# Optimization experiments

Measured on AMD Instinct MI355X. Metric: run time of the kernel, lower is better.

The kernel has to match this reference:

```python
import jax, jax.numpy as jnp
import numpy as np

N = 50000      # nodes
E = 800000     # edges (avg degree 16)
DIN = 128
DH = 128
DOUT = 8


def setup_inputs() -> dict:
    key = jax.random.key(0)
    ks = jax.random.split(key, 9)
    def lin(k, o, i):
        return (jax.random.normal(k, (o, i), jnp.float32) / np.sqrt(i)).astype(jnp.float32)
    return {
        "x": jax.random.normal(ks[0], (N, DIN), jnp.float32),
        "edge_index": jax.random.randint(ks[1], (2, E), 0, N),
        "edge_attr": jax.random.normal(ks[2], (E, 1), jnp.float32),
        # SAGEConv params: lin_l (applied to mean-aggregated neighbors, with bias)
        # and lin_r (applied to root node, no bias), per PyG defaults.
        "W1l": lin(ks[3], DH, DIN), "b1l": jnp.zeros((DH,), jnp.float32), "W1r": lin(ks[4], DH, DIN),
        "Whl": lin(ks[5], DH, DH),  "bhl": jnp.zeros((DH,), jnp.float32), "Whr": lin(ks[6], DH, DH),
        "W2l": lin(ks[7], DOUT, DH), "b2l": jnp.zeros((DOUT,), jnp.float32), "W2r": lin(ks[8], DOUT, DH),
    }


def _sage_conv(x, src, dst, Wl, bl, Wr, n):
    # mean aggregation of source features onto destination nodes
    s = jax.ops.segment_sum(x[src], dst, num_segments=n)              # [N, d]
    c = jax.ops.segment_sum(jnp.ones((src.shape[0],), x.dtype), dst, num_segments=n)
    agg = s / jnp.maximum(c, 1.0)[:, None]
    return agg @ Wl.T + bl + x @ Wr.T


def reference(x, edge_index, edge_attr, W1l, b1l, W1r, Whl, bhl, Whr, W2l, b2l, W2r):
    # edge_attr is accepted but unused, matching the original forward.
    src, dst = edge_index[0], edge_index[1]
    n = x.shape[0]
    h = jax.nn.relu(_sage_conv(x, src, dst, W1l, b1l, W1r, n))
    # dropout p=0.5 is identity at inference (training=False)
    h = jax.nn.elu(_sage_conv(h, src, dst, Whl, bhl, Whr, n))
    h = _sage_conv(h, src, dst, W2l, b2l, W2r, n)
    return jax.nn.log_softmax(h, axis=1)
```

## Files before the change

### kernel.cpp

```cpp
#include <hip/hip_runtime.h>

typedef unsigned int u32;
typedef unsigned short u16;
typedef short bf16x8 __attribute__((ext_vector_type(8)));
typedef float f32x4 __attribute__((ext_vector_type(4)));

#define NCB 256

__device__ __forceinline__ float bf2f(u16 h) { return __uint_as_float(((u32)h) << 16); }
__device__ __forceinline__ u16 f2bf(float f) {
    u32 u = __float_as_uint(f);
    return (u16)((u + 0x7fffu + ((u >> 16) & 1u)) >> 16);
}

__global__ __launch_bounds__(256) void k_sentinel(u16* out, int n) {
    int i = blockIdx.x * 256 + threadIdx.x;
    if (i < n) out[i] = f2bf(-7.0f);
}

__global__ void k_detect(const u32* x, int* flag) {
    int lane = threadIdx.x;
    int c = 0;
    for (int j = 0; j < 4; ++j) {
        u32 u = x[lane * 4 + j];
        u32 e = (u >> 7) & 0xffu;
        if ((e >= 0x30u && e <= 0x47u) || ((u & 0x7fffu) == 0u)) ++c;
    }
    for (int d = 32; d; d >>= 1) c += __shfl_down(c, d, 64);
    if (lane == 0) *flag = (c < 128) ? 1 : 0;
}

__global__ __launch_bounds__(256) void k_front(
    const void* x, const int* dstv, const int* flag, int bucketed,
    uint4* X, int* C, int E, int N, int chunk, int cvtB,
    const void* s1l, const void* s1r, const void* shl, const void* shr,
    const void* s2l, const void* s2r, const void* sb1, const void* sbh,
    const void* sb2,
    u32* w1l, u32* w1r, u32* whl, u32* whr, u32* w2l, u32* w2r,
    float* bf1, float* bfh, float* bf2) {
    __shared__ int hist[256];
    int b = blockIdx.x, t = threadIdx.x;
    if (b < cvtB) {
        int i = b * 256 + t;
        if (i >= N * 16) return;
        if (*flag) {
            const float4* s = (const float4*)x;
            float4 a = s[2 * i], c4 = s[2 * i + 1];
            uint4 o;
            o.x = (u32)f2bf(a.x) | ((u32)f2bf(a.y) << 16);
            o.y = (u32)f2bf(a.z) | ((u32)f2bf(a.w) << 16);
            o.z = (u32)f2bf(c4.x) | ((u32)f2bf(c4.y) << 16);
            o.w = (u32)f2bf(c4.z) | ((u32)f2bf(c4.w) << 16);
            X[i] = o;
        } else {
            X[i] = ((const uint4*)x)[i];
        }
    } else if (b < cvtB + 134) {
        int bb = b - cvtB;
        int fl = *flag;
        auto cv = [&](const void* src, u32* dst, int base) {
            int i = base + t;
            if (fl) {
                const float* s = (const float*)src;
                dst[i] = (u32)f2bf(s[2 * i]) | ((u32)f2bf(s[2 * i + 1]) << 16);
            } else {
                dst[i] = ((const u32*)src)[i];
            }
        };
        auto cb = [&](const void* src, float* dst, int i) {
            dst[i] = fl ? ((const float*)src)[i] : bf2f(((const u16*)src)[i]);
        };
        if      (bb <  32) cv(s1l, w1l, bb * 256);
        else if (bb <  64) cv(s1r, w1r, (bb - 32) * 256);
        else if (bb <  96) cv(shl, whl, (bb - 64) * 256);
        else if (bb < 128) cv(shr, whr, (bb - 96) * 256);
        else if (bb < 130) cv(s2l, w2l, (bb - 128) * 256);
        else if (bb < 132) cv(s2r, w2r, (bb - 130) * 256);
        else if (bb == 132) {
            if (t < 128) cb(sb1, bf1, t);
            else         cb(sbh, bfh, t - 128);
        } else {
            if (t < 8) cb(sb2, bf2, t);
        }
    } else if (bucketed) {
        int cb2 = b - cvtB - 134;
        hist[t] = 0;
        __syncthreads();
        int e0 = cb2 * chunk;
        int e1 = min(e0 + chunk, E);
        for (int e = e0 + t; e < e1; e += 256) {
            int d = min(max(dstv[e], 0), N - 1);
            atomicAdd(&hist[d >> 8], 1);
        }
        __syncthreads();
        C[cb2 * 256 + t] = hist[t];
    }
}

__global__ __launch_bounds__(256) void k_scanT(int* C, int* T) {
    __shared__ int sm[256];
    int bu = blockIdx.x, t = threadIdx.x;
    int v = C[t * 256 + bu];
    sm[t] = v;
    __syncthreads();
    for (int off = 1; off < 256; off <<= 1) {
        int u = (t >= off) ? sm[t - off] : 0;
        __syncthreads();
        sm[t] += u;
        __syncthreads();
    }
    C[t * 256 + bu] = sm[t] - v;
    if (t == 255) T[bu] = sm[255];
}

__global__ __launch_bounds__(256) void k_scanB(const int* T, int* B, int nbuk) {
    __shared__ int sm[256];
    int t = threadIdx.x;
    int v = (t < nbuk) ? T[t] : 0;
    sm[t] = v;
    __syncthreads();
    for (int off = 1; off < 256; off <<= 1) {
        int u = (t >= off) ? sm[t - off] : 0;
        __syncthreads();
        sm[t] += u;
        __syncthreads();
    }
    B[t] = sm[t] - v;
}

__global__ __launch_bounds__(256) void k_place(const int* srcv, const int* dstv,
                                               const int* C, const int* Bb,
                                               u32* pairs, int E, int N, int chunk) {
    __shared__ int base[256], cnt[256];
    int t = threadIdx.x;
    base[t] = Bb[t] + C[blockIdx.x * 256 + t];
    cnt[t] = 0;
    __syncthreads();
    int e0 = blockIdx.x * chunk;
    int e1 = min(e0 + chunk, E);
    for (int e = e0 + t; e < e1; e += 256) {
        int d = min(max(dstv[e], 0), N - 1);
        int s = min(max(srcv[e], 0), N - 1);
        int b = d >> 8;
        int pos = base[b] + atomicAdd(&cnt[b], 1);
        pos = min(max(pos, 0), E - 1);
        pairs[pos] = ((u32)s << 8) | (u32)(d & 255);
    }
}

__global__ __launch_bounds__(256) void k_fillb2(const u32* pairs, const int* Bb,
                                                const int* T, int* rowptr,
                                                int* adj, int E, int N, int nbuk) {
    int bu = blockIdx.x;
    int n0 = bu << 8;
    int nn = min(N - n0, 256);
    __shared__ int dcnt[256], sm[256], cur[256];
    int t = threadIdx.x;
    dcnt[t] = 0;
    __syncthreads();
    int s0 = min(max(Bb[bu], 0), E);
    int s1 = min(s0 + max(T[bu], 0), E);
    for (int e = s0 + t; e < s1; e += 256) {
        int ld = (int)(pairs[e] & 255u);
        atomicAdd(&dcnt[min(ld, nn - 1)], 1);
    }
    __syncthreads();
    int v = dcnt[t];
    sm[t] = v;
    __syncthreads();
    for (int off = 1; off < 256; off <<= 1) {
        int u = (t >= off) ? sm[t - off] : 0;
        __syncthreads();
        sm[t] += u;
        __syncthreads();
    }
    int excl = sm[t] - v;
    cur[t] = excl;
    if (t < nn) rowptr[n0 + t] = s0 + excl;
    if (bu == nbuk - 1 && t == 0) rowptr[N] = E;
    __syncthreads();
    for (int e = s0 + t; e < s1; e += 256) {
        u32 pc = pairs[e];
        int ld = min((int)(pc & 255u), nn - 1);
        int src = (int)(pc >> 8);
        int slot = atomicAdd(&cur[ld], 1);
        int idx = min(max(s0 + slot, 0), E - 1);
        adj[idx] = src;
    }
}

__global__ __launch_bounds__(256) void k_zero(int* deg, int N) {
    int i = blockIdx.x * 256 + threadIdx.x;
    if (i < N) deg[i] = 0;
}
__global__ __launch_bounds__(256) void k_deg(const int* dstv, int* deg, int E, int N) {
    int e = blockIdx.x * 256 + threadIdx.x;
    if (e >= E) return;
    int d = dstv[e]; d = min(max(d, 0), N - 1);
    atomicAdd(&deg[d], 1);
}
__global__ __launch_bounds__(512) void k_scan1(const int* deg, int* r0,
                                               int* bsums, int N) {
    __shared__ int sm[512];
    int i = blockIdx.x * 512 + threadIdx.x;
    int v = (i < N) ? deg[i] : 0;
    sm[threadIdx.x] = v;
    __syncthreads();
    for (int off = 1; off < 512; off <<= 1) {
        int t = (threadIdx.x >= off) ? sm[threadIdx.x - off] : 0;
        __syncthreads();
        sm[threadIdx.x] += t;
        __syncthreads();
    }
    if (i < N) r0[i] = sm[threadIdx.x] - v;
    if (threadIdx.x == 511) bsums[blockIdx.x] = sm[511];
}
__global__ __launch_bounds__(128) void k_scan2f(int* bsums, int nb) {
    __shared__ int sm[128];
    int v = (threadIdx.x < nb) ? bsums[threadIdx.x] : 0;
    sm[threadIdx.x] = v;
    __syncthreads();
    for (int off = 1; off < 128; off <<= 1) {
        int t = (threadIdx.x >= off) ? sm[threadIdx.x - off] : 0;
        __syncthreads();
        sm[threadIdx.x] += t;
        __syncthreads();
    }
    if (threadIdx.x < nb) bsums[threadIdx.x] = sm[threadIdx.x] - v;
}
__global__ __launch_bounds__(512) void k_scan3f(const int* r0, const int* bsums,
                                                int* rowptr, int N, int E) {
    int i = blockIdx.x * 512 + threadIdx.x;
    if (i < N) rowptr[i] = r0[i] + bsums[blockIdx.x];
    if (i == 0) rowptr[N] = E;
}
__global__ __launch_bounds__(256) void k_fill(const int* srcv, const int* dstv,
                                              const int* rowptr, int* deg,
                                              int* adj, int E, int N) {
    int e = blockIdx.x * 256 + threadIdx.x;
    if (e >= E) return;
    int d = dstv[e]; d = min(max(d, 0), N - 1);
    int slot = atomicSub(&deg[d], 1) - 1;
    int idx = rowptr[d] + slot;
    idx = min(max(idx, 0), E - 1);
    adj[idx] = srcv[e];
}

__device__ __forceinline__ void acc8m(uint4 u, float m, float* s) {
    const u32* pu = (const u32*)&u;
#pragma unroll
    for (int t = 0; t < 4; ++t) {
        s[2 * t]     = fmaf(__uint_as_float(pu[t] << 16), m, s[2 * t]);
        s[2 * t + 1] = fmaf(__uint_as_float(pu[t] & 0xffff0000u), m, s[2 * t + 1]);
    }
}

__global__ __launch_bounds__(256) void k_aggregate(const uint4* F, const int* rowptr,
                                                   const int* adj, uint4* A,
                                                   int N, int E) {
    int wid = (int)((blockIdx.x * 256u + threadIdx.x) >> 6);
    int lane = threadIdx.x & 63;
    if (wid >= N) return;
    int beg = rowptr[wid], end = rowptr[wid + 1];
    beg = min(max(beg, 0), E);
    end = min(max(end, beg), E);
    int g = lane >> 4, l = lane & 15;
    float s[8] = {0.f, 0.f, 0.f, 0.f, 0.f, 0.f, 0.f, 0.f};
    for (int j = beg + g; j < end; j += 16) {
        int i1 = j + 4, i2 = j + 8, i3 = j + 12;
        float m1 = (i1 < end) ? 1.f : 0.f;
        float m2 = (i2 < end) ? 1.f : 0.f;
        float m3 = (i3 < end) ? 1.f : 0.f;
        int a0 = min(max(adj[j], 0), N - 1);
        int a1 = min(max(adj[min(i1, end - 1)], 0), N - 1);
        int a2 = min(max(adj[min(i2, end - 1)], 0), N - 1);
        int a3 = min(max(adj[min(i3, end - 1)], 0), N - 1);
        uint4 u0 = F[(size_t)a0 * 16 + l];
        uint4 u1 = F[(size_t)a1 * 16 + l];
        uint4 u2 = F[(size_t)a2 * 16 + l];
        uint4 u3 = F[(size_t)a3 * 16 + l];
        acc8m(u0, 1.f, s);
        acc8m(u1, m1, s);
        acc8m(u2, m2, s);
        acc8m(u3, m3, s);
    }
#pragma unroll
    for (int k = 0; k < 8; ++k) {
        s[k] += __shfl_xor(s[k], 16, 64);
        s[k] += __shfl_xor(s[k], 32, 64);
    }
    if (g == 0) {
        float inv = 1.f / fmaxf((float)(end - beg), 1.f);
        uint4 r; u32* pr = (u32*)&r;
#pragma unroll
        for (int t = 0; t < 4; ++t)
            pr[t] = (u32)f2bf(s[2 * t] * inv) | ((u32)f2bf(s[2 * t + 1] * inv) << 16);
        A[(size_t)wid * 16 + l] = r;
    }
}

__global__ __launch_bounds__(256) void k_gemm128(const u16* Agg, const u16* Xin,
                                                 const u32* Wl, const u32* Wr,
                                                 const float* bias, u16* Out, int N) {
    __shared__ __align__(16) u16 Wsh[32768];
    int t = threadIdx.x;
#pragma unroll
    for (int i = 0; i < 16; ++i) {
        int f = i * 256 + t;
        int c = f >> 9, s = (f >> 6) & 7, q = (f >> 4) & 3, n = f & 15;
        int o = c * 16 + n;
        int k = s * 32 + q * 8;
        uint4 v;
        if (k < 128) v = *(const uint4*)(Wl + (size_t)o * 64 + (k >> 1));
        else         v = *(const uint4*)(Wr + (size_t)o * 64 + ((k - 128) >> 1));
        *(uint4*)(Wsh + f * 8) = v;
    }
    __syncthreads();

    int tile = blockIdx.x * 4 + (t >> 6);
    int lane = t & 63;
    int m0 = tile * 16;
    if (m0 >= N) return;
    int mrow = min(m0 + (lane & 15), N - 1);
    int kq = (lane >> 4) * 8;

    bf16x8 afrag[8];
#pragma unroll
    for (int s = 0; s < 8; ++s) {
        int k = s * 32 + kq;
        const u16* p = (k < 128) ? (Agg + (size_t)mrow * 128 + k)
                                 : (Xin + (size_t)mrow * 128 + (k - 128));
        afrag[s] = *(const bf16x8*)p;
    }

    f32x4 acc[8];
#pragma unroll
    for (int c = 0; c < 8; ++c) acc[c] = (f32x4){0.f, 0.f, 0.f, 0.f};

    const u16* lbase = Wsh + (lane >> 4) * 128 + (lane & 15) * 8;
#pragma unroll
    for (int c = 0; c < 8; ++c) {
#pragma unroll
        for (int s = 0; s < 8; ++s) {
            bf16x8 b = *(const bf16x8*)(lbase + (c * 8 + s) * 512);
            acc[c] = __builtin_amdgcn_mfma_f32_16x16x32_bf16(afrag[s], b, acc[c], 0, 0, 0);
        }
    }

#pragma unroll
    for (int c = 0; c < 8; ++c) {
        int o = c * 16 + (lane & 15);
        float bv = bias[o];
#pragma unroll
        for (int r = 0; r < 4; ++r) {
            int m = m0 + (lane >> 4) * 4 + r;
            float v = acc[c][r] + bv;
            v = fmaxf(v, 0.f);
            if (m < N) Out[(size_t)m * 128 + o] = f2bf(v);
        }
    }
}

__global__ __launch_bounds__(256) void k_gemm2(const u16* Agg, const u16* Xin,
                                               const u32* Wl, const u32* Wr,
                                               const float* bias,
                                               const u32* W2l, const u32* W2r,
                                               const float* b2,
                                               float* Y, float* R, int N) {
    __shared__ __align__(16) u16 Wsh[32768];
    __shared__ float W2sh[2048];
    int t = threadIdx.x;
#pragma unroll
    for (int i = 0; i < 16; ++i) {
        int f = i * 256 + t;
        int c = f >> 9, s = (f >> 6) & 7, q = (f >> 4) & 3, n = f & 15;
        int o = c * 16 + n;
        int k = s * 32 + q * 8;
        uint4 v;
        if (k < 128) v = *(const uint4*)(Wl + (size_t)o * 64 + (k >> 1));
        else         v = *(const uint4*)(Wr + (size_t)o * 64 + ((k - 128) >> 1));
        *(uint4*)(Wsh + f * 8) = v;
    }
#pragma unroll
    for (int i = t; i < 512; i += 256) {
        u32 wa = W2l[i], wb = W2r[i];
        W2sh[2 * i]            = bf2f((u16)(wa & 0xffffu));
        W2sh[2 * i + 1]        = bf2f((u16)(wa >> 16));
        W2sh[1024 + 2 * i]     = bf2f((u16)(wb & 0xffffu));
        W2sh[1024 + 2 * i + 1] = bf2f((u16)(wb >> 16));
    }
    __syncthreads();

    int tile = blockIdx.x * 4 + (t >> 6);
    int lane = t & 63;
    int m0 = tile * 16;
    if (m0 >= N) return;
    int mrow = min(m0 + (lane & 15), N - 1);
    int kq = (lane >> 4) * 8;

    bf16x8 afrag[8];
#pragma unroll
    for (int s = 0; s < 8; ++s) {
        int k = s * 32 + kq;
        const u16* p = (k < 128) ? (Agg + (size_t)mrow * 128 + k)
                                 : (Xin + (size_t)mrow * 128 + (k - 128));
        afrag[s] = *(const bf16x8*)p;
    }

    f32x4 acc[8];
#pragma unroll
    for (int c = 0; c < 8; ++c) acc[c] = (f32x4){0.f, 0.f, 0.f, 0.f};

    const u16* lbase = Wsh + (lane >> 4) * 128 + (lane & 15) * 8;
#pragma unroll
    for (int c = 0; c < 8; ++c) {
#pragma unroll
        for (int s = 0; s < 8; ++s) {
            bf16x8 b = *(const bf16x8*)(lbase + (c * 8 + s) * 512);
            acc[c] = __builtin_amdgcn_mfma_f32_16x16x32_bf16(afrag[s], b, acc[c], 0, 0, 0);
        }
    }

    int quad = lane >> 4, k15 = lane & 15;
#pragma unroll
    for (int c = 0; c < 8; ++c) {
        float bv = bias[c * 16 + k15];
#pragma unroll
        for (int r = 0; r < 4; ++r) {
            float v = acc[c][r] + bv;
            acc[c][r] = (v > 0.f) ? v : expm1f(v);
        }
    }
#pragma unroll
    for (int j = 0; j < 8; ++j) {
        float py[4] = {0.f, 0.f, 0.f, 0.f};
        float pr[4] = {0.f, 0.f, 0.f, 0.f};
#pragma unroll
        for (int c = 0; c < 8; ++c) {
            float w1 = W2sh[j * 128 + c * 16 + k15];
            float w2 = W2sh[1024 + j * 128 + c * 16 + k15];
#pragma unroll
            for (int r = 0; r < 4; ++r) {
                py[r] = fmaf(acc[c][r], w1, py[r]);
                pr[r] = fmaf(acc[c][r], w2, pr[r]);
            }
        }
#pragma unroll
        for (int r = 0; r < 4; ++r) {
#pragma unroll
            for (int d = 1; d < 16; d <<= 1) {
                py[r] += __shfl_xor(py[r], d, 64);
                pr[r] += __shfl_xor(pr[r], d, 64);
            }
            int m = m0 + quad * 4 + r;
            if (k15 == j && m < N) {
                Y[(size_t)m * 8 + j] = py[r];
                R[(size_t)m * 8 + j] = pr[r] + b2[j];
            }
        }
    }
}

__global__ __launch_bounds__(256) void k_agg8sm(const float* Y, const float* R,
                                                const int* rowptr, const int* adj,
                                                const int* flag, void* Out,
                                                int N, int E) {
    int t = blockIdx.x * 256 + threadIdx.x;
    int n = t >> 3;
    int o = t & 7;
    if (n >= N) return;
    int beg = rowptr[n], end = rowptr[n + 1];
    beg = min(max(beg, 0), E);
    end = min(max(end, beg), E);
    float s = 0.f;
    int j = beg;
    for (; j + 1 < end; j += 2) {
        int a0 = min(max(adj[j], 0), N - 1);
        int a1 = min(max(adj[j + 1], 0), N - 1);
        s += Y[(size_t)a0 * 8 + o];
        s += Y[(size_t)a1 * 8 + o];
    }
    if (j < end) {
        int a0 = min(max(adj[j], 0), N - 1);
        s += Y[(size_t)a0 * 8 + o];
    }
    float acc = s / fmaxf((float)(end - beg), 1.f) + R[(size_t)n * 8 + o];
    float mx = acc;
#pragma unroll
    for (int d = 1; d < 8; d <<= 1) mx = fmaxf(mx, __shfl_xor(mx, d, 64));
    float ex = expf(acc - mx), se = ex;
#pragma unroll
    for (int d = 1; d < 8; d <<= 1) se += __shfl_xor(se, d, 64);
    float v = acc - mx - logf(se);
    if (*flag) ((float*)Out)[(size_t)n * 8 + o] = v;
    else       ((u16*)Out)[(size_t)n * 8 + o] = f2bf(v);
}

extern "C" void kernel_launch(void* const* d_in, const int* in_sizes, int n_in,
                              void* d_out, int out_size, void* d_ws, size_t ws_size,
                              hipStream_t stream) {
    const void* x   = d_in[0];
    const int* ei   = (const int*)d_in[1];
    const int N = in_sizes[0] / 128;
    const int E = in_sizes[1] / 2;
    const int* srcv = ei;
    const int* dstv = ei + E;
    const int NBUK = (N + 255) >> 8;
    const int bucketed = (NBUK <= 256) ? 1 : 0;
    const int chunk = (E + NCB - 1) / NCB;
    const int cvtB = (N * 16 + 255) / 256;
    const int nbA = (N + 511) / 512;

    auto rnd = [](size_t b) { return (b + 255) & ~(size_t)255; };
    size_t need = rnd(256)
                + rnd((size_t)N * 4)
                + rnd((size_t)N * 4)
                + rnd((size_t)(N + 1) * 4)
                + rnd(4096)
                + rnd(256 * NCB * 4)
                + rnd(1024) + rnd(1024)
                + rnd((size_t)E * 4)
                + 2 * rnd((size_t)N * 256)
                + 2 * rnd((size_t)N * 32)
                + 4 * rnd(32768) + 2 * rnd(2048) + 2 * rnd(512) + rnd(64);
    if (ws_size < need) {
        k_sentinel<<<(out_size + 255) / 256, 256, 0, stream>>>((u16*)d_out, out_size);
        return;
    }

    char* p = (char*)d_ws;
    auto carve = [&](size_t bytes) { char* r = p; p += (bytes + 255) & ~(size_t)255; return r; };
    int* flag   = (int*)carve(256);
    int* deg    = (int*)carve((size_t)N * 4);
    int* r0     = (int*)carve((size_t)N * 4);
    int* rowptr = (int*)carve((size_t)(N + 1) * 4);
    int* bsums  = (int*)carve(4096);
    int* C      = (int*)carve(256 * NCB * 4);
    int* T      = (int*)carve(1024);
    int* B      = (int*)carve(1024);
    int* adj    = (int*)carve((size_t)E * 4);
    u32* X      = (u32*)carve((size_t)N * 256);
    u32* A      = (u32*)carve((size_t)N * 256);
    float* Y    = (float*)carve((size_t)N * 32);
    float* R    = (float*)carve((size_t)N * 32);
    u32* w1l = (u32*)carve(32768); u32* w1r = (u32*)carve(32768);
    u32* whl = (u32*)carve(32768); u32* whr = (u32*)carve(32768);
    u32* w2l = (u32*)carve(2048);  u32* w2r = (u32*)carve(2048);
    float* bf1 = (float*)carve(512); float* bfh = (float*)carve(512);
    float* bf2 = (float*)carve(64);
    u32* pairs = A;
    (void)n_in;

    k_detect<<<1, 64, 0, stream>>>((const u32*)x, flag);
    k_front<<<cvtB + 134 + (bucketed ? 256 : 0), 256, 0, stream>>>(
        x, dstv, flag, bucketed, (uint4*)X, C, E, N, chunk, cvtB,
        d_in[3], d_in[5], d_in[6], d_in[8], d_in[9], d_in[11],
        d_in[4], d_in[7], d_in[10],
        w1l, w1r, whl, whr, w2l, w2r, bf1, bfh, bf2);
    if (bucketed) {
        k_scanT<<<NBUK, 256, 0, stream>>>(C, T);
        k_scanB<<<1, 256, 0, stream>>>(T, B, NBUK);
        k_place<<<NCB, 256, 0, stream>>>(srcv, dstv, C, B, pairs, E, N, chunk);
        k_fillb2<<<NBUK, 256, 0, stream>>>(pairs, B, T, rowptr, adj, E, N, NBUK);
    } else {
        k_zero<<<(N + 255) / 256, 256, 0, stream>>>(deg, N);
        k_deg<<<(E + 255) / 256, 256, 0, stream>>>(dstv, deg, E, N);
        k_scan1<<<nbA, 512, 0, stream>>>(deg, r0, bsums, N);
        k_scan2f<<<1, 128, 0, stream>>>(bsums, nbA);
        k_scan3f<<<nbA, 512, 0, stream>>>(r0, bsums, rowptr, N, E);
        k_fill<<<(E + 255) / 256, 256, 0, stream>>>(srcv, dstv, rowptr, deg, adj, E, N);
    }

    int aggBlocks = (int)(((size_t)N * 64 + 255) / 256);
    int gemmBlocks = ((N + 15) / 16 + 3) / 4;
    int perNode8 = (int)(((size_t)N * 8 + 255) / 256);

    k_aggregate<<<aggBlocks, 256, 0, stream>>>((const uint4*)X, rowptr, adj, (uint4*)A, N, E);
    k_gemm128<<<gemmBlocks, 256, 0, stream>>>((const u16*)A, (const u16*)X, w1l, w1r, bf1, (u16*)X, N);
    k_aggregate<<<aggBlocks, 256, 0, stream>>>((const uint4*)X, rowptr, adj, (uint4*)A, N, E);
    k_gemm2<<<gemmBlocks, 256, 0, stream>>>((const u16*)A, (const u16*)X, whl, whr, bfh,
                                            w2l, w2r, bf2, Y, R, N);
    k_agg8sm<<<perNode8, 256, 0, stream>>>(Y, R, rowptr, adj, flag, d_out, N, E);
}
```

Measured before the change: 257.3 us.

## Merge GEMM kernels into a persistent templated kernel with A-tile prefetch

Replaces the two one-tile-per-warp GEMM kernels with one templated kernel launched as a fixed grid of 512 blocks. Each warp loops over many 16-row tiles and loads the next tile's A fragments while the MFMAs for the current tile run. Because far fewer blocks are launched, the 64KB weight staging into LDS is paid fewer times. The final 8-output projection now uses a butterfly shuffle reduction instead of 8 separate full 16-lane reductions. The risks are higher register pressure (prefetch buffers plus 64 partial sums under launch_bounds 256,2, which may spill) and less parallelism from the smaller fixed grid.

```diff
diff --git a/kernel.cpp b/kernel.cpp
--- a/kernel.cpp
+++ b/kernel.cpp
@@ -6,6 +6,7 @@
 typedef float f32x4 __attribute__((ext_vector_type(4)));
 
 #define NCB 256
+#define GEMM_BLOCKS 512
 
 __device__ __forceinline__ float bf2f(u16 h) { return __uint_as_float(((u32)h) << 16); }
 __device__ __forceinline__ u16 f2bf(float f) {
@@ -299,10 +300,37 @@
     }
 }
 
-__global__ __launch_bounds__(256) void k_gemm128(const u16* Agg, const u16* Xin,
-                                                 const u32* Wl, const u32* Wr,
-                                                 const float* bias, u16* Out, int N) {
+__device__ __forceinline__ float bfly8(const float* v, int r, bool b0, bool b1, bool b2) {
+    float w0[4];
+#pragma unroll
+    for (int jj = 0; jj < 4; ++jj) {
+        float snd = b0 ? v[jj * 4 + r] : v[(jj + 4) * 4 + r];
+        float rec = __shfl_xor(snd, 1, 64);
+        w0[jj] = (b0 ? v[(jj + 4) * 4 + r] : v[jj * 4 + r]) + rec;
+    }
+    float w1v[2];
+#pragma unroll
+    for (int kk = 0; kk < 2; ++kk) {
+        float snd = b1 ? w1v[0] * 0.f + w0[kk] : w0[kk + 2];
+        snd = b1 ? w0[kk] : w0[kk + 2];
+        float rec = __shfl_xor(snd, 2, 64);
+        w1v[kk] = (b1 ? w0[kk + 2] : w0[kk]) + rec;
+    }
+    float snd = b2 ? w1v[0] : w1v[1];
+    float rec = __shfl_xor(snd, 4, 64);
+    float w2v = (b2 ? w1v[1] : w1v[0]) + rec;
+    w2v += __shfl_xor(w2v, 8, 64);
+    return w2v;
+}
+
+template <int LAYER>
+__global__ __launch_bounds__(256, 2) void k_gemmP(
+    const u16* Agg, const u16* Xin, const u32* Wl, const u32* Wr,
+    const float* bias, u16* OutX,
+    const u32* W2l, const u32* W2r, const float* b2p,
+    float* Y, float* R, int N) {
     __shared__ __align__(16) u16 Wsh[32768];
+    __shared__ float W2sh[(LAYER == 1) ? 2048 : 4];
     int t = threadIdx.x;
 #pragma unroll
     for (int i = 0; i < 16; ++i) {
@@ -315,149 +343,113 @@
         else         v = *(const uint4*)(Wr + (size_t)o * 64 + ((k - 128) >> 1));
         *(uint4*)(Wsh + f * 8) = v;
     }
-    __syncthreads();
-
-    int tile = blockIdx.x * 4 + (t >> 6);
+    if (LAYER == 1) {
+#pragma unroll
+        for (int i = t; i < 512; i += 256) {
+            u32 wa = W2l[i], wb = W2r[i];
+            W2sh[2 * i]            = bf2f((u16)(wa & 0xffffu));
+            W2sh[2 * i + 1]        = bf2f((u16)(wa >> 16));
+            W2sh[1024 + 2 * i]     = bf2f((u16)(wb & 0xffffu));
+            W2sh[1024 + 2 * i + 1] = bf2f((u16)(wb >> 16));
+        }
+    }
+    __syncthreads();
+
     int lane = t & 63;
-    int m0 = tile * 16;
-    if (m0 >= N) return;
-    int mrow = min(m0 + (lane & 15), N - 1);
-    int kq = (lane >> 4) * 8;
-
-    bf16x8 afrag[8];
-#pragma unroll
-    for (int s = 0; s < 8; ++s) {
-        int k = s * 32 + kq;
-        const u16* p = (k < 128) ? (Agg + (size_t)mrow * 128 + k)
-                                 : (Xin + (size_t)mrow * 128 + (k - 128));
-        afrag[s] = *(const bf16x8*)p;
-    }
-
-    f32x4 acc[8];
-#pragma unroll
-    for (int c = 0; c < 8; ++c) acc[c] = (f32x4){0.f, 0.f, 0.f, 0.f};
-
-    const u16* lbase = Wsh + (lane >> 4) * 128 + (lane & 15) * 8;
-#pragma unroll
-    for (int c = 0; c < 8; ++c) {
+    int wid = t >> 6;
+    int quad = lane >> 4, k15 = lane & 15;
+    int kq = quad * 8;
+    int ntiles = (N + 15) >> 4;
+    int tstride = gridDim.x * 4;
+    int tile = blockIdx.x * 4 + wid;
+    const u16* lbase = Wsh + quad * 128 + k15 * 8;
+
+    auto loadA = [&](bf16x8* fr, int tl) {
+        int mrow = min(tl * 16 + k15, N - 1);
 #pragma unroll
         for (int s = 0; s < 8; ++s) {
-            bf16x8 b = *(const bf16x8*)(lbase + (c * 8 + s) * 512);
-            acc[c] = __builtin_amdgcn_mfma_f32_16x16x32_bf16(afrag[s], b, acc[c], 0, 0, 0);
-        }
-    }
-
-#pragma unroll
-    for (int c = 0; c < 8; ++c) {
-        int o = c * 16 + (lane & 15);
-        float bv = bias[o];
-#pragma unroll
-        for (int r = 0; r < 4; ++r) {
-            int m = m0 + (lane >> 4) * 4 + r;
-            float v = acc[c][r] + bv;
-            v = fmaxf(v, 0.f);
-            if (m < N) Out[(size_t)m * 128 + o] = f2bf(v);
-        }
-    }
-}
-
-__global__ __launch_bounds__(256) void k_gemm2(const u16* Agg, const u16* Xin,
-                                               const u32* Wl, const u32* Wr,
-                                               const float* bias,
-                                               const u32* W2l, const u32* W2r,
-                                               const float* b2,
-                                               float* Y, float* R, int N) {
-    __shared__ __align__(16) u16 Wsh[32768];
-    __shared__ float W2sh[2048];
-    int t = threadIdx.x;
-#pragma unroll
-    for (int i = 0; i < 16; ++i) {
-        int f = i * 256 + t;
-        int c = f >> 9, s = (f >> 6) & 7, q = (f >> 4) & 3, n = f & 15;
-        int o = c * 16 + n;
-        int k = s * 32 + q * 8;
-        uint4 v;
-        if (k < 128) v = *(const uint4*)(Wl + (size_t)o * 64 + (k >> 1));
-        else         v = *(const uint4*)(Wr + (size_t)o * 64 + ((k - 128) >> 1));
-        *(uint4*)(Wsh + f * 8) = v;
-    }
-#pragma unroll
-    for (int i = t; i < 512; i += 256) {
-        u32 wa = W2l[i], wb = W2r[i];
-        W2sh[2 * i]            = bf2f((u16)(wa & 0xffffu));
-        W2sh[2 * i + 1]        = bf2f((u16)(wa >> 16));
-        W2sh[1024 + 2 * i]     = bf2f((u16)(wb & 0xffffu));
-        W2sh[1024 + 2 * i + 1] = bf2f((u16)(wb >> 16));
-    }
-    __syncthreads();
-
-    int tile = blockIdx.x * 4 + (t >> 6);
-    int lane = t & 63;
-    int m0 = tile * 16;
-    if (m0 >= N) return;
-    int mrow = min(m0 + (lane & 15), N - 1);
-    int kq = (lane >> 4) * 8;
-
-    bf16x8 afrag[8];
-#pragma unroll
-    for (int s = 0; s < 8; ++s) {
-        int k = s * 32 + kq;
-        const u16* p = (k < 128) ? (Agg + (size_t)mrow * 128 + k)
-                                 : (Xin + (size_t)mrow * 128 + (k - 128));
-        afrag[s] = *(const bf16x8*)p;
-    }
-
-    f32x4 acc[8];
-#pragma unroll
-    for (int c = 0; c < 8; ++c) acc[c] = (f32x4){0.f, 0.f, 0.f, 0.f};
-
-    const u16* lbase = Wsh + (lane >> 4) * 128 + (lane & 15) * 8;
-#pragma unroll
-    for (int c = 0; c < 8; ++c) {
-#pragma unroll
-        for (int s = 0; s < 8; ++s) {
-            bf16x8 b = *(const bf16x8*)(lbase + (c * 8 + s) * 512);
-            acc[c] = __builtin_amdgcn_mfma_f32_16x16x32_bf16(afrag[s], b, acc[c], 0, 0, 0);
-        }
-    }
-
-    int quad = lane >> 4, k15 = lane & 15;
-#pragma unroll
-    for (int c = 0; c < 8; ++c) {
-        float bv = bias[c * 16 + k15];
-#pragma unroll
-        for (int r = 0; r < 4; ++r) {
-            float v = acc[c][r] + bv;
-            acc[c][r] = (v > 0.f) ? v : expm1f(v);
-        }
-    }
-#pragma unroll
-    for (int j = 0; j < 8; ++j) {
-        float py[4] = {0.f, 0.f, 0.f, 0.f};
-        float pr[4] = {0.f, 0.f, 0.f, 0.f};
+            int k = s * 32 + kq;
+            const u16* p = (k < 128) ? (Agg + (size_t)mrow * 128 + k)
+                                     : (Xin + (size_t)mrow * 128 + (k - 128));
+            fr[s] = *(const bf16x8*)p;
+        }
+    };
+
+    bf16x8 curA[8];
+    if (tile < ntiles) loadA(curA, tile);
+
+    for (; tile < ntiles; tile += tstride) {
+        int nt = tile + tstride;
+        bf16x8 nxtA[8];
+        loadA(nxtA, (nt < ntiles) ? nt : tile);
+
+        f32x4 acc[8];
+#pragma unroll
+        for (int c = 0; c < 8; ++c) acc[c] = (f32x4){0.f, 0.f, 0.f, 0.f};
 #pragma unroll
         for (int c = 0; c < 8; ++c) {
-            float w1 = W2sh[j * 128 + c * 16 + k15];
-            float w2 = W2sh[1024 + j * 128 + c * 16 + k15];
+#pragma unroll
+            for (int s = 0; s < 8; ++s) {
+                bf16x8 b = *(const bf16x8*)(lbase + (c * 8 + s) * 512);
+                acc[c] = __builtin_amdgcn_mfma_f32_16x16x32_bf16(curA[s], b, acc[c], 0, 0, 0);
+            }
+        }
+
+        int m0 = tile * 16;
+        if (LAYER == 0) {
+#pragma unroll
+            for (int c = 0; c < 8; ++c) {
+                int o = c * 16 + k15;
+                float bv = bias[o];
+#pragma unroll
+                for (int r = 0; r < 4; ++r) {
+                    int m = m0 + quad * 4 + r;
+                    float v = acc[c][r] + bv;
+                    v = fmaxf(v, 0.f);
+                    if (m < N) OutX[(size_t)m * 128 + o] = f2bf(v);
+                }
+            }
+        } else {
+#pragma unroll
+            for (int c = 0; c < 8; ++c) {
+                float bv = bias[c * 16 + k15];
+#pragma unroll
+                for (int r = 0; r < 4; ++r) {
+                    float v = acc[c][r] + bv;
+                    acc[c][r] = (v > 0.f) ? v : expm1f(v);
+                }
+            }
+            float py[32], pr[32];
+#pragma unroll
+            for (int i = 0; i < 32; ++i) { py[i] = 0.f; pr[i] = 0.f; }
+#pragma unroll
+            for (int j = 0; j < 8; ++j) {
+#pragma unroll
+                for (int c = 0; c < 8; ++c) {
+                    float w1 = W2sh[j * 128 + c * 16 + k15];
+                    float w2 = W2sh[1024 + j * 128 + c * 16 + k15];
+#pragma unroll
+                    for (int r = 0; r < 4; ++r) {
+                        py[j * 4 + r] = fmaf(acc[c][r], w1, py[j * 4 + r]);
+                        pr[j * 4 + r] = fmaf(acc[c][r], w2, pr[j * 4 + r]);
+                    }
+                }
+            }
+            bool bb0 = (k15 & 1) != 0, bb1 = (k15 & 2) != 0, bb2 = (k15 & 4) != 0;
+            int jmine = 4 * (k15 & 1) + (k15 & 2) + ((k15 >> 2) & 1);
 #pragma unroll
             for (int r = 0; r < 4; ++r) {
-                py[r] = fmaf(acc[c][r], w1, py[r]);
-                pr[r] = fmaf(acc[c][r], w2, pr[r]);
+                float yv = bfly8(py, r, bb0, bb1, bb2);
+                float rv = bfly8(pr, r, bb0, bb1, bb2);
+                int m = m0 + quad * 4 + r;
+                if (m < N) {
+                    if (k15 < 8) Y[(size_t)m * 8 + jmine] = yv;
+                    else         R[(size_t)m * 8 + jmine] = rv + b2p[jmine];
+                }
             }
         }
 #pragma unroll
-        for (int r = 0; r < 4; ++r) {
-#pragma unroll
-            for (int d = 1; d < 16; d <<= 1) {
-                py[r] += __shfl_xor(py[r], d, 64);
-                pr[r] += __shfl_xor(pr[r], d, 64);
-            }
-            int m = m0 + quad * 4 + r;
-            if (k15 == j && m < N) {
-                Y[(size_t)m * 8 + j] = py[r];
-                R[(size_t)m * 8 + j] = pr[r] + b2[j];
-            }
-        }
+        for (int s = 0; s < 8; ++s) curA[s] = nxtA[s];
     }
 }
 
@@ -572,13 +564,14 @@
     }
 
     int aggBlocks = (int)(((size_t)N * 64 + 255) / 256);
-    int gemmBlocks = ((N + 15) / 16 + 3) / 4;
     int perNode8 = (int)(((size_t)N * 8 + 255) / 256);
 
     k_aggregate<<<aggBlocks, 256, 0, stream>>>((const uint4*)X, rowptr, adj, (uint4*)A, N, E);
-    k_gemm128<<<gemmBlocks, 256, 0, stream>>>((const u16*)A, (const u16*)X, w1l, w1r, bf1, (u16*)X, N);
+    k_gemmP<0><<<GEMM_BLOCKS, 256, 0, stream>>>((const u16*)A, (const u16*)X, w1l, w1r,
+                                                bf1, (u16*)X, nullptr, nullptr, nullptr,
+                                                nullptr, nullptr, N);
     k_aggregate<<<aggBlocks, 256, 0, stream>>>((const uint4*)X, rowptr, adj, (uint4*)A, N, E);
-    k_gemm2<<<gemmBlocks, 256, 0, stream>>>((const u16*)A, (const u16*)X, whl, whr, bfh,
-                                            w2l, w2r, bf2, Y, R, N);
+    k_gemmP<1><<<GEMM_BLOCKS, 256, 0, stream>>>((const u16*)A, (const u16*)X, whl, whr,
+                                                bfh, nullptr, w2l, w2r, bf2, Y, R, N);
     k_agg8sm<<<perNode8, 256, 0, stream>>>(Y, R, rowptr, adj, flag, d_out, N, E);
 }
```

Result: slower. 529.4 us (+105.8%).
